# Kernel tuning notes

Hardware: AMD Instinct MI355X
Metric: run time of the kernel (lower is better)

The kernel has to match this reference:

```python
import jax, jax.numpy as jnp
import numpy as np
import math

INV = 1.0 / (2.0 * math.pi) ** 2  # 1/(2*pi)^2 normalization used throughout
EPS = 1e-8


def setup_inputs() -> dict:
    key = jax.random.key(0)
    ks = jax.random.split(key, 5)
    N, K, J = 512, 8, 6
    return {
        "x_hat": jax.random.normal(ks[0], (N, N, 2), jnp.float32),
        "phi_hat_real": jax.random.normal(ks[1], (N, N), jnp.float32),
        "phi_hat_imag": jax.random.normal(ks[2], (N, N), jnp.float32),
        "psi_hat_real": jax.random.normal(ks[3], (K, J, N, N), jnp.float32),
        "psi_hat_imag": jax.random.normal(ks[4], (K, J, N, N), jnp.float32),
    }


def reference(x_hat, phi_hat_real, phi_hat_imag, psi_hat_real, psi_hat_imag):
    K, J, N, _ = psi_hat_real.shape
    NN = N * N
    phi2 = phi_hat_real ** 2 + phi_hat_imag ** 2  # [N,N]

    # zeroth-order coefficient: full spatial mean of |x_hat|^2 * |phi_hat|^2
    s0 = INV * jnp.mean((x_hat[:, :, 0] ** 2 + x_hat[:, :, 1] ** 2) * phi2)

    # first layer: complex multiply in Fourier domain, ifft2, modulus, fft2
    xc = jax.lax.complex(x_hat[:, :, 0], x_hat[:, :, 1])          # [N,N] complex
    psic = jax.lax.complex(psi_hat_real, psi_hat_imag)            # [K,J,N,N] complex
    temp = jnp.fft.ifft2(xc[None, None] * psic, axes=(-2, -1))    # [K,J,N,N] complex
    mod = jnp.sqrt(temp.real ** 2 + temp.imag ** 2 + EPS)         # modulus nonlinearity
    t2 = jnp.fft.fft2(mod, axes=(-2, -1))                         # rfft onesided=False == full fft of real
    power = (t2.real ** 2 + t2.imag ** 2).reshape(K, J, NN)       # |U1_hat|^2

    # first-order coefficients a[k,i] = INV * mean(power * phi2)
    a = INV * (power @ phi2.reshape(NN)) / NN                     # [K,J]

    # second-order coefficients via GEMM over spatial dim:
    # B[k,i,m,j] = INV * mean_xy(power[k,i] * |psi[m,j]|^2)
    psi2 = (psi_hat_real ** 2 + psi_hat_imag ** 2).reshape(K, J, NN)
    B = INV * jnp.einsum('kin,mjn->kimj', power, psi2) / NN       # [K,J,K,J]

    # assemble output in the same concatenation order as the torch loop:
    # [s0, a_0, b_0(flattened over k,m,j'), a_1, b_1, ..., a_{J-1}]
    pieces = [s0[None]]
    for i in range(J):
        pieces.append(a[:, i])
        if i < J - 1:
            pieces.append(B[:, i, :, i + 1:J].reshape(-1))
    return jnp.concatenate(pieces, axis=0)
```

## Files before the change

kernel.cpp:

```cpp
#include <hip/hip_runtime.h>
#include <hip/hip_fp16.h>

#define Nn 512
#define NNe 262144
#define CST 546

__device__ __forceinline__ float2 f2(float x, float y){ return make_float2(x, y); }
__device__ __forceinline__ float2 cadd(float2 a, float2 b){ return f2(a.x+b.x, a.y+b.y); }
__device__ __forceinline__ float2 csub(float2 a, float2 b){ return f2(a.x-b.x, a.y-b.y); }
__device__ __forceinline__ float2 cmul(float2 a, float2 b){
    return f2(a.x*b.x - a.y*b.y, a.x*b.y + a.y*b.x);
}
__device__ __forceinline__ int pidx(int p){ return p + (p>>4) + (p>>7); }
#define WFENCE() __builtin_amdgcn_wave_barrier()

template<int SGN>
__device__ __forceinline__ void fft8(float2 a[8]){
    const float r = 0.7071067811865476f;
    const float S = (float)SGN;
    float2 u0 = cadd(a[0], a[4]), u1 = cadd(a[1], a[5]);
    float2 u2 = cadd(a[2], a[6]), u3 = cadd(a[3], a[7]);
    float2 v0 = csub(a[0], a[4]), v1 = csub(a[1], a[5]);
    float2 v2 = csub(a[2], a[6]), v3 = csub(a[3], a[7]);
    v1 = cmul(v1, f2(r, S*r));
    v2 = cmul(v2, f2(0.f, S));
    v3 = cmul(v3, f2(-r, S*r));
    float2 p0 = cadd(u0, u2), p1 = cadd(u1, u3);
    float2 q0 = csub(u0, u2), q1 = cmul(csub(u1, u3), f2(0.f, S));
    a[0] = cadd(p0, p1); a[4] = csub(p0, p1);
    a[2] = cadd(q0, q1); a[6] = csub(q0, q1);
    p0 = cadd(v0, v2); p1 = cadd(v1, v3);
    q0 = csub(v0, v2); q1 = cmul(csub(v1, v3), f2(0.f, S));
    a[1] = cadd(p0, p1); a[5] = csub(p0, p1);
    a[3] = cadd(q0, q1); a[7] = csub(q0, q1);
}

__device__ __forceinline__ float2 twdp(int idx, float inv){
    float ang = 6.283185307179586f * (inv * (float)idx);
    float s, c;
    __sincosf(ang, &s, &c);
    return f2(c, s);
}

template<int SGN>
__device__ void fft512_dif_i(float2 v[8], float2* buf, int lane){
    fft8<SGN>(v);
    {
        float2 w1 = twdp(lane, 1.f/512.f);
        if (SGN < 0) w1.y = -w1.y;
        float2 w  = f2(1.f, 0.f);
        #pragma unroll
        for (int r = 0; r < 8; ++r){
            buf[pidx(r*64 + lane)] = cmul(v[r], w);
            w = cmul(w, w1);
        }
    }
    WFENCE();
    int rb = (lane >> 3) * 64, t2 = lane & 7;
    float2 y[8];
    #pragma unroll
    for (int q = 0; q < 8; ++q) y[q] = buf[pidx(rb + t2 + 8*q)];
    fft8<SGN>(y);
    WFENCE();
    {
        float2 w2 = twdp(t2, 1.f/64.f);
        if (SGN < 0) w2.y = -w2.y;
        float2 w  = f2(1.f, 0.f);
        #pragma unroll
        for (int r = 0; r < 8; ++r){
            buf[pidx(rb + r*8 + t2)] = cmul(y[r], w);
            w = cmul(w, w2);
        }
    }
    WFENCE();
    int base = rb + t2*8;
    #pragma unroll
    for (int q = 0; q < 8; ++q) v[q] = buf[pidx(base + q)];
    fft8<SGN>(v);
}

template<int SGN>
__device__ void fft512_dit_i(float2 v[8], float2* buf, int lane){
    int rb = (lane >> 3) * 64, t2 = lane & 7;
    fft8<SGN>(v);
    int base = rb + t2*8;
    #pragma unroll
    for (int q = 0; q < 8; ++q) buf[pidx(base + q)] = v[q];
    WFENCE();
    float2 y[8];
    #pragma unroll
    for (int r = 0; r < 8; ++r) y[r] = buf[pidx(rb + r*8 + t2)];
    {
        float2 w2 = twdp(t2, 1.f/64.f);
        if (SGN < 0) w2.y = -w2.y;
        float2 w  = f2(1.f, 0.f);
        #pragma unroll
        for (int r = 0; r < 8; ++r){
            y[r] = cmul(y[r], w);
            w = cmul(w, w2);
        }
    }
    fft8<SGN>(y);
    WFENCE();
    #pragma unroll
    for (int q = 0; q < 8; ++q) buf[pidx(rb + t2 + 8*q)] = y[q];
    WFENCE();
    #pragma unroll
    for (int r = 0; r < 8; ++r) v[r] = buf[pidx(r*64 + lane)];
    {
        float2 w1 = twdp(lane, 1.f/512.f);
        if (SGN < 0) w1.y = -w1.y;
        float2 w  = f2(1.f, 0.f);
        #pragma unroll
        for (int r = 0; r < 8; ++r){
            v[r] = cmul(v[r], w);
            w = cmul(w, w1);
        }
    }
    fft8<SGN>(v);
}

__global__ __launch_bounds__(256, 6)
void k_mulrow(const float2* __restrict__ xh, const float* __restrict__ pr,
              const float* __restrict__ pi, __half2* __restrict__ temp,
              __half* __restrict__ psi2h){
    __shared__ float2 lds[4][548];
    int wave = threadIdx.x >> 6, lane = threadIdx.x & 63;
    int img  = blockIdx.x >> 7;
    int row  = ((blockIdx.x & 127) << 2) | wave;
    size_t boff = (size_t)img * NNe + (size_t)row * Nn;
    const float2* xr = xh + (size_t)row * Nn;
    float2 v[8];
    #pragma unroll
    for (int q = 0; q < 8; ++q){
        int x = lane + 64*q;
        float2 xv = xr[x];
        float2 pv = f2(pr[boff + x], pi[boff + x]);
        psi2h[boff + x] = __float2half_rn(pv.x*pv.x + pv.y*pv.y);
        v[q] = cmul(xv, pv);
    }
    fft512_dif_i<1>(v, lds[wave], lane);
    __half2* outp = temp + boff;
    #pragma unroll
    for (int q = 0; q < 8; ++q) outp[64*q + lane] = __floats2half2_rn(v[q].x, v[q].y);
}

__global__ __launch_bounds__(512, 2)
void k_colfused(__half2* __restrict__ temp){
    __shared__ __half2 st[16][521];
    __shared__ float2 fbuf[8][CST];
    int img = blockIdx.x >> 5;
    int x0  = (blockIdx.x & 31) << 4;
    __half2* src = temp + (size_t)img * NNe + x0;
    for (int i = threadIdx.x; i < 2048; i += 512){
        int row = i >> 2, c4 = (i & 3) << 2;
        uint4 u = *(const uint4*)&src[(size_t)row * Nn + c4];
        st[c4+0][row] = *(__half2*)&u.x;
        st[c4+1][row] = *(__half2*)&u.y;
        st[c4+2][row] = *(__half2*)&u.z;
        st[c4+3][row] = *(__half2*)&u.w;
    }
    __syncthreads();
    int wave = threadIdx.x >> 6, lane = threadIdx.x & 63;
    const float sc = 3.814697265625e-06f;
    float2* buf = fbuf[wave];
    int c0 = 2*wave, c1 = c0 + 1;
    float2 a[8], b[8];
    #pragma unroll
    for (int q = 0; q < 8; ++q) a[q] = __half22float2(st[c0][lane + 64*q]);
    fft512_dif_i<1>(a, buf, lane);
    WFENCE();
    #pragma unroll
    for (int q = 0; q < 8; ++q) b[q] = __half22float2(st[c1][lane + 64*q]);
    fft512_dif_i<1>(b, buf, lane);
    float2 z[8];
    #pragma unroll
    for (int q = 0; q < 8; ++q){
        float r0 = a[q].x*sc, i0 = a[q].y*sc;
        float r1 = b[q].x*sc, i1 = b[q].y*sc;
        z[q] = f2(sqrtf(r0*r0 + i0*i0 + 1e-8f), sqrtf(r1*r1 + i1*i1 + 1e-8f));
    }
    WFENCE();
    fft512_dit_i<-1>(z, buf, lane);
    #pragma unroll
    for (int q = 0; q < 8; ++q) buf[pidx(lane + 64*q)] = z[q];
    WFENCE();
    #pragma unroll
    for (int q = 0; q < 8; ++q){
        int k = lane + 64*q;
        float2 zr = buf[pidx((512 - k) & 511)];
        float2 zv = z[q];
        st[c0][k] = __floats2half2_rn(0.5f*(zv.x + zr.x), 0.5f*(zv.y - zr.y));
        st[c1][k] = __floats2half2_rn(0.5f*(zv.y + zr.y), 0.5f*(zr.x - zv.x));
    }
    __syncthreads();
    for (int i = threadIdx.x; i < 2048; i += 512){
        int row = i >> 2, c4 = (i & 3) << 2;
        uint4 u;
        *(__half2*)&u.x = st[c4+0][row];
        *(__half2*)&u.y = st[c4+1][row];
        *(__half2*)&u.z = st[c4+2][row];
        *(__half2*)&u.w = st[c4+3][row];
        *(uint4*)&src[(size_t)row * Nn + c4] = u;
    }
}

__global__ __launch_bounds__(256, 6)
void k_rowpow(const __half2* __restrict__ temp, __half* __restrict__ powerh){
    __shared__ float2 lds[4][548];
    int wave = threadIdx.x >> 6, lane = threadIdx.x & 63;
    int img  = blockIdx.x >> 7;
    int row  = ((blockIdx.x & 127) << 2) | wave;
    const __half2* src = temp + (size_t)img * NNe + (size_t)row * Nn;
    float2 v[8];
    #pragma unroll
    for (int q = 0; q < 8; ++q) v[q] = __half22float2(src[64*q + lane]);
    fft512_dit_i<-1>(v, lds[wave], lane);
    __half* dst = powerh + (size_t)img * NNe + (size_t)row * Nn;
    #pragma unroll
    for (int q = 0; q < 8; ++q)
        dst[lane + 64*q] = __float2half_rn((v[q].x*v[q].x + v[q].y*v[q].y) * 0.00390625f);
}

__global__ __launch_bounds__(256)
void k_s0(const float2* __restrict__ xh, const float* __restrict__ phr,
          const float* __restrict__ phii, float* __restrict__ part){
    int gid = blockIdx.x*256 + threadIdx.x;
    float acc = 0.f;
    for (int n = gid; n < NNe; n += 256*256){
        float2 x = xh[n];
        float a = phr[n], b = phii[n];
        acc += (x.x*x.x + x.y*x.y) * (a*a + b*b);
    }
    #pragma unroll
    for (int o = 32; o > 0; o >>= 1) acc += __shfl_down(acc, o, 64);
    __shared__ float wsum[4];
    int wave = threadIdx.x >> 6, lane = threadIdx.x & 63;
    if (lane == 0) wsum[wave] = acc;
    __syncthreads();
    if (threadIdx.x == 0) part[blockIdx.x] = wsum[0]+wsum[1]+wsum[2]+wsum[3];
}

__global__ __launch_bounds__(128)
void k_gemm(const __half* __restrict__ powerh, const __half* __restrict__ psi2h,
            const float* __restrict__ phr, const float* __restrict__ phii,
            float* __restrict__ partC){
    __shared__ __align__(16) float P[2][48][68];
    __shared__ __align__(16) float W[2][56][68];
    int wave = threadIdx.x >> 6, lane = threadIdx.x & 63;
    float (*Pw)[68] = P[wave];
    float (*Ww)[68] = W[wave];
    int gw = blockIdx.x*2 + wave;
    int lm = lane >> 3, lw = lane & 7;
    float acc[6][7] = {};
    #pragma unroll
    for (int r = 49; r < 56; ++r){
        Ww[r][lane] = 0.f;
        if (lane < 4) Ww[r][64 + lane] = 0.f;
    }
    int n0 = gw * 256;
    for (int st = 0; st < 4; ++st){
        int nb = n0 + st*64;
        WFENCE();
        #pragma unroll
        for (int rr = 0; rr < 12; ++rr){
            int row = rr*4 + (lane >> 4);
            int c4  = (lane & 15) * 4;
            size_t off = (size_t)row*NNe + nb + c4;
            const __half2* p2 = (const __half2*)&powerh[off];
            float2 f0 = __half22float2(p2[0]);
            float2 f1 = __half22float2(p2[1]);
            *(float4*)&Pw[row][c4] = make_float4(f0.x, f0.y, f1.x, f1.y);
        }
        #pragma unroll
        for (int rr = 0; rr < 12; ++rr){
            int row = rr*4 + (lane >> 4);
            int c4  = (lane & 15) * 4;
            size_t off = (size_t)row*NNe + nb + c4;
            const __half2* p2 = (const __half2*)&psi2h[off];
            float2 f0 = __half22float2(p2[0]);
            float2 f1 = __half22float2(p2[1]);
            *(float4*)&Ww[row][c4] = make_float4(f0.x, f0.y, f1.x, f1.y);
        }
        if (lane < 16){
            int c4 = lane * 4;
            float4 a = *(const float4*)&phr[nb + c4];
            float4 b = *(const float4*)&phii[nb + c4];
            float4 w4;
            w4.x = a.x*a.x + b.x*b.x; w4.y = a.y*a.y + b.y*b.y;
            w4.z = a.z*a.z + b.z*b.z; w4.w = a.w*a.w + b.w*b.w;
            *(float4*)&Ww[48][c4] = w4;
        }
        WFENCE();
        #pragma unroll 2
        for (int nn = 0; nn < 64; nn += 4){
            float4 pa[6], wb[7];
            #pragma unroll
            for (int i = 0; i < 6; ++i) pa[i] = *(const float4*)&Pw[lm + 8*i][nn];
            #pragma unroll
            for (int j = 0; j < 7; ++j) wb[j] = *(const float4*)&Ww[lw + 8*j][nn];
            #pragma unroll
            for (int i = 0; i < 6; ++i)
                #pragma unroll
                for (int j = 0; j < 7; ++j){
                    float s = acc[i][j];
                    s = fmaf(pa[i].x, wb[j].x, s);
                    s = fmaf(pa[i].y, wb[j].y, s);
                    s = fmaf(pa[i].z, wb[j].z, s);
                    s = fmaf(pa[i].w, wb[j].w, s);
                    acc[i][j] = s;
                }
        }
    }
    float* outp = partC + (size_t)gw * 2400;
    #pragma unroll
    for (int i = 0; i < 6; ++i)
        #pragma unroll
        for (int j = 0; j < 7; ++j){
            int m = lm + 8*i, wc = lw + 8*j;
            if (wc < 49) outp[m*50 + wc] = acc[i][j];
        }
}

__global__ __launch_bounds__(256)
void k_redc1(const float* __restrict__ partC, float* __restrict__ partC2){
    __shared__ float red[4][64];
    int es = threadIdx.x & 63, wave = threadIdx.x >> 6;
    int e = blockIdx.x*64 + es;
    int b0 = blockIdx.y*64 + wave*16;
    float s = 0.f;
    if (e < 2400){
        #pragma unroll
        for (int u = 0; u < 16; ++u) s += partC[(size_t)(b0+u)*2400 + e];
    }
    red[wave][es] = s;
    __syncthreads();
    if (wave == 0 && e < 2400)
        partC2[(size_t)blockIdx.y*2400 + e] = red[0][es]+red[1][es]+red[2][es]+red[3][es];
}

__global__ __launch_bounds__(256)
void k_final(const float* __restrict__ partC2, const float* __restrict__ partS0,
             float* __restrict__ outp, float SC0, float SCC){
    __shared__ float CFs[2400];
    __shared__ float ssum[4];
    int tid = threadIdx.x, wave = tid >> 6, lane = tid & 63;
    for (int e = tid; e < 2400; e += 256){
        float s = 0.f;
        #pragma unroll
        for (int u = 0; u < 16; ++u) s += partC2[(size_t)u*2400 + e];
        CFs[e] = SCC * s;
    }
    float a = partS0[tid];
    #pragma unroll
    for (int o = 32; o > 0; o >>= 1) a += __shfl_down(a, o, 64);
    if (lane == 0) ssum[wave] = a;
    __syncthreads();
    if (tid == 0) outp[0] = SC0 * (ssum[0]+ssum[1]+ssum[2]+ssum[3]);
    int off = 1;
    for (int i = 0; i < 6; ++i){
        if (tid < 8) outp[off + tid] = CFs[(tid*6 + i)*50 + 48];
        off += 8;
        if (i < 5){
            int nj = 5 - i, cnt = 64 * nj;
            for (int p = tid; p < cnt; p += 256){
                int j2 = p % nj;
                int km = p / nj;
                int m = km & 7, k = km >> 3;
                outp[off + p] = CFs[(k*6 + i)*50 + m*6 + (i + 1 + j2)];
            }
            off += cnt;
        }
    }
}

extern "C" void kernel_launch(void* const* d_in, const int* in_sizes, int n_in,
                              void* d_out, int out_size, void* d_ws, size_t ws_size,
                              hipStream_t stream){
    (void)in_sizes; (void)n_in; (void)out_size; (void)ws_size;
    const float2* xh  = (const float2*)d_in[0];
    const float*  phr = (const float*)d_in[1];
    const float*  phi_= (const float*)d_in[2];
    const float*  psr = (const float*)d_in[3];
    const float*  psi_= (const float*)d_in[4];
    float* outp = (float*)d_out;
    float* ws   = (float*)d_ws;

    size_t o_power = 0;
    size_t o_partC = o_power + (size_t)24 * NNe;
    size_t o_pC2   = o_partC + (size_t)1024 * 2400;
    size_t o_s0    = o_pC2 + (size_t)16 * 2400;
    size_t o_temp  = o_s0 + 256;
    size_t o_psi2  = o_temp + (size_t)48 * NNe;
    __half*  powerh= (__half*)(ws + o_power);
    float*   partC = ws + o_partC;
    float*   partC2= ws + o_pC2;
    float*   ps0   = ws + o_s0;
    __half2* temp  = (__half2*)(ws + o_temp);
    __half*  psi2h = (__half*)(ws + o_psi2);

    const double INVd = 1.0 / (4.0 * 3.14159265358979323846 * 3.14159265358979323846);
    const float SC0 = (float)(INVd / (double)NNe);
    const float SCC = (float)(INVd / (double)NNe * 256.0);

    k_s0<<<dim3(256), dim3(256), 0, stream>>>(xh, phr, phi_, ps0);
    k_mulrow<<<dim3(48*128), dim3(256), 0, stream>>>(xh, psr, psi_, temp, psi2h);
    k_colfused<<<dim3(48*32), dim3(512), 0, stream>>>(temp);
    k_rowpow<<<dim3(48*128), dim3(256), 0, stream>>>(temp, powerh);
    k_gemm<<<dim3(512), dim3(128), 0, stream>>>(powerh, psi2h, phr, phi_, partC);
    k_redc1<<<dim3(38, 16), dim3(256), 0, stream>>>(partC, partC2);
    k_final<<<dim3(1), dim3(256), 0, stream>>>(partC2, ps0, outp, SC0, SCC);
}
```

Baseline: 140.1 us.

## Alias column-FFT scratch onto transpose tile to cut LDS and raise occupancy

The column kernel previously held two separate shared buffers: a half2 transpose tile and per-wave float2 FFT scratch. It now uses one shared region that serves as the transpose tile and is reused as FFT scratch after the column data is loaded into registers. New FFT variants use a smaller p2idx padding (stride 520) so the scratch fits, and launch bounds go from 2 to 3 blocks per CU. This adds extra block-wide barriers and keeps more values in registers, which may raise register pressure, and the new padding scheme may bring bank conflicts.

```diff
diff --git a/kernel.cpp b/kernel.cpp
--- a/kernel.cpp
+++ b/kernel.cpp
@@ -4,6 +4,8 @@
 #define Nn 512
 #define NNe 262144
 #define CST 546
+#define SST 521
+#define FST 520
 
 __device__ __forceinline__ float2 f2(float x, float y){ return make_float2(x, y); }
 __device__ __forceinline__ float2 cadd(float2 a, float2 b){ return f2(a.x+b.x, a.y+b.y); }
@@ -12,6 +14,7 @@
     return f2(a.x*b.x - a.y*b.y, a.x*b.y + a.y*b.x);
 }
 __device__ __forceinline__ int pidx(int p){ return p + (p>>4) + (p>>7); }
+__device__ __forceinline__ int p2idx(int p){ return p + (p>>6); }
 #define WFENCE() __builtin_amdgcn_wave_barrier()
 
 template<int SGN>
@@ -120,6 +123,84 @@
     fft8<SGN>(v);
 }
 
+template<int SGN>
+__device__ void fft512_dif_s(float2 v[8], float2* buf, int lane){
+    fft8<SGN>(v);
+    {
+        float2 w1 = twdp(lane, 1.f/512.f);
+        if (SGN < 0) w1.y = -w1.y;
+        float2 w  = f2(1.f, 0.f);
+        #pragma unroll
+        for (int r = 0; r < 8; ++r){
+            buf[p2idx(r*64 + lane)] = cmul(v[r], w);
+            w = cmul(w, w1);
+        }
+    }
+    WFENCE();
+    int rb = (lane >> 3) * 64, t2 = lane & 7;
+    float2 y[8];
+    #pragma unroll
+    for (int q = 0; q < 8; ++q) y[q] = buf[p2idx(rb + t2 + 8*q)];
+    fft8<SGN>(y);
+    WFENCE();
+    {
+        float2 w2 = twdp(t2, 1.f/64.f);
+        if (SGN < 0) w2.y = -w2.y;
+        float2 w  = f2(1.f, 0.f);
+        #pragma unroll
+        for (int r = 0; r < 8; ++r){
+            buf[p2idx(rb + r*8 + t2)] = cmul(y[r], w);
+            w = cmul(w, w2);
+        }
+    }
+    WFENCE();
+    int base = rb + t2*8;
+    #pragma unroll
+    for (int q = 0; q < 8; ++q) v[q] = buf[p2idx(base + q)];
+    fft8<SGN>(v);
+}
+
+template<int SGN>
+__device__ void fft512_dit_s(float2 v[8], float2* buf, int lane){
+    int rb = (lane >> 3) * 64, t2 = lane & 7;
+    fft8<SGN>(v);
+    int base = rb + t2*8;
+    #pragma unroll
+    for (int q = 0; q < 8; ++q) buf[p2idx(base + q)] = v[q];
+    WFENCE();
+    float2 y[8];
+    #pragma unroll
+    for (int r = 0; r < 8; ++r) y[r] = buf[p2idx(rb + r*8 + t2)];
+    {
+        float2 w2 = twdp(t2, 1.f/64.f);
+        if (SGN < 0) w2.y = -w2.y;
+        float2 w  = f2(1.f, 0.f);
+        #pragma unroll
+        for (int r = 0; r < 8; ++r){
+            y[r] = cmul(y[r], w);
+            w = cmul(w, w2);
+        }
+    }
+    fft8<SGN>(y);
+    WFENCE();
+    #pragma unroll
+    for (int q = 0; q < 8; ++q) buf[p2idx(rb + t2 + 8*q)] = y[q];
+    WFENCE();
+    #pragma unroll
+    for (int r = 0; r < 8; ++r) v[r] = buf[p2idx(r*64 + lane)];
+    {
+        float2 w1 = twdp(lane, 1.f/512.f);
+        if (SGN < 0) w1.y = -w1.y;
+        float2 w  = f2(1.f, 0.f);
+        #pragma unroll
+        for (int r = 0; r < 8; ++r){
+            v[r] = cmul(v[r], w);
+            w = cmul(w, w1);
+        }
+    }
+    fft8<SGN>(v);
+}
+
 __global__ __launch_bounds__(256, 6)
 void k_mulrow(const float2* __restrict__ xh, const float* __restrict__ pr,
               const float* __restrict__ pi, __half2* __restrict__ temp,
@@ -145,34 +226,35 @@
     for (int q = 0; q < 8; ++q) outp[64*q + lane] = __floats2half2_rn(v[q].x, v[q].y);
 }
 
-__global__ __launch_bounds__(512, 2)
+__global__ __launch_bounds__(512, 3)
 void k_colfused(__half2* __restrict__ temp){
-    __shared__ __half2 st[16][521];
-    __shared__ float2 fbuf[8][CST];
+    __shared__ __align__(16) unsigned char smem[16 * SST * 4];
+    __half2* st   = (__half2*)smem;
     int img = blockIdx.x >> 5;
     int x0  = (blockIdx.x & 31) << 4;
     __half2* src = temp + (size_t)img * NNe + x0;
     for (int i = threadIdx.x; i < 2048; i += 512){
         int row = i >> 2, c4 = (i & 3) << 2;
         uint4 u = *(const uint4*)&src[(size_t)row * Nn + c4];
-        st[c4+0][row] = *(__half2*)&u.x;
-        st[c4+1][row] = *(__half2*)&u.y;
-        st[c4+2][row] = *(__half2*)&u.z;
-        st[c4+3][row] = *(__half2*)&u.w;
+        st[(c4+0)*SST + row] = *(__half2*)&u.x;
+        st[(c4+1)*SST + row] = *(__half2*)&u.y;
+        st[(c4+2)*SST + row] = *(__half2*)&u.z;
+        st[(c4+3)*SST + row] = *(__half2*)&u.w;
     }
     __syncthreads();
     int wave = threadIdx.x >> 6, lane = threadIdx.x & 63;
-    const float sc = 3.814697265625e-06f;
-    float2* buf = fbuf[wave];
     int c0 = 2*wave, c1 = c0 + 1;
     float2 a[8], b[8];
     #pragma unroll
-    for (int q = 0; q < 8; ++q) a[q] = __half22float2(st[c0][lane + 64*q]);
-    fft512_dif_i<1>(a, buf, lane);
-    WFENCE();
-    #pragma unroll
-    for (int q = 0; q < 8; ++q) b[q] = __half22float2(st[c1][lane + 64*q]);
-    fft512_dif_i<1>(b, buf, lane);
+    for (int q = 0; q < 8; ++q) a[q] = __half22float2(st[c0*SST + lane + 64*q]);
+    #pragma unroll
+    for (int q = 0; q < 8; ++q) b[q] = __half22float2(st[c1*SST + lane + 64*q]);
+    __syncthreads();
+    float2* buf = (float2*)smem + wave * FST;
+    const float sc = 3.814697265625e-06f;
+    fft512_dif_s<1>(a, buf, lane);
+    WFENCE();
+    fft512_dif_s<1>(b, buf, lane);
     float2 z[8];
     #pragma unroll
     for (int q = 0; q < 8; ++q){
@@ -181,26 +263,34 @@
         z[q] = f2(sqrtf(r0*r0 + i0*i0 + 1e-8f), sqrtf(r1*r1 + i1*i1 + 1e-8f));
     }
     WFENCE();
-    fft512_dit_i<-1>(z, buf, lane);
-    #pragma unroll
-    for (int q = 0; q < 8; ++q) buf[pidx(lane + 64*q)] = z[q];
-    WFENCE();
+    fft512_dit_s<-1>(z, buf, lane);
+    #pragma unroll
+    for (int q = 0; q < 8; ++q) buf[p2idx(lane + 64*q)] = z[q];
+    WFENCE();
+    float2 zr[8];
+    #pragma unroll
+    for (int q = 0; q < 8; ++q) zr[q] = buf[p2idx((512 - (lane + 64*q)) & 511)];
+    __half2 m0[8], m1[8];
     #pragma unroll
     for (int q = 0; q < 8; ++q){
-        int k = lane + 64*q;
-        float2 zr = buf[pidx((512 - k) & 511)];
-        float2 zv = z[q];
-        st[c0][k] = __floats2half2_rn(0.5f*(zv.x + zr.x), 0.5f*(zv.y - zr.y));
-        st[c1][k] = __floats2half2_rn(0.5f*(zv.y + zr.y), 0.5f*(zr.x - zv.x));
+        float2 zv = z[q], w = zr[q];
+        m0[q] = __floats2half2_rn(0.5f*(zv.x + w.x), 0.5f*(zv.y - w.y));
+        m1[q] = __floats2half2_rn(0.5f*(zv.y + w.y), 0.5f*(w.x - zv.x));
+    }
+    __syncthreads();
+    #pragma unroll
+    for (int q = 0; q < 8; ++q){
+        st[c0*SST + lane + 64*q] = m0[q];
+        st[c1*SST + lane + 64*q] = m1[q];
     }
     __syncthreads();
     for (int i = threadIdx.x; i < 2048; i += 512){
         int row = i >> 2, c4 = (i & 3) << 2;
         uint4 u;
-        *(__half2*)&u.x = st[c4+0][row];
-        *(__half2*)&u.y = st[c4+1][row];
-        *(__half2*)&u.z = st[c4+2][row];
-        *(__half2*)&u.w = st[c4+3][row];
+        *(__half2*)&u.x = st[(c4+0)*SST + row];
+        *(__half2*)&u.y = st[(c4+1)*SST + row];
+        *(__half2*)&u.z = st[(c4+2)*SST + row];
+        *(__half2*)&u.w = st[(c4+3)*SST + row];
         *(uint4*)&src[(size_t)row * Nn + c4] = u;
     }
 }
```

New measurement: 141.3 us. About the same (+0.8%).
